# Kernel tuning notes

Hardware: AMD Instinct MI355X
Metric: run time of the kernel (lower is better)

The kernel has to match this reference:

```python
import jax, jax.numpy as jnp
import numpy as np

N_HEADS = 16

def setup_inputs() -> dict:
    key = jax.random.key(0)
    ks = jax.random.split(key, 5)
    B, T, D, L = 2, 2048, 1024, 128
    x = jax.random.normal(ks[0], (B, T, D), dtype=jnp.float32)
    w_q = jax.random.normal(ks[1], (D, D), dtype=jnp.float32) / np.sqrt(D)
    w_d = jax.random.normal(ks[2], (D, L), dtype=jnp.float32) / np.sqrt(D)
    w_k = jax.random.normal(ks[3], (L, D), dtype=jnp.float32) / np.sqrt(L)
    w_v = jax.random.normal(ks[4], (L, D), dtype=jnp.float32) / np.sqrt(L)
    mask = jnp.ones((B, T), dtype=jnp.int32)
    return {"x": x, "mask": mask, "w_q": w_q, "w_d": w_d, "w_k": w_k, "w_v": w_v}


def reference(x, mask, w_q, w_d, w_k, w_v):
    B, T, D = x.shape
    H = N_HEADS
    dh = D // H
    q = x @ w_q                      # [B,T,D]
    latent = x @ w_d                 # [B,T,L]
    k = latent @ w_k                 # [B,T,D]
    v = latent @ w_v                 # [B,T,D]

    def split(t):
        return t.reshape(B, T, H, dh).transpose(0, 2, 1, 3)  # [B,H,T,dh]

    q, k, v = split(q), split(k), split(v)
    scores = jnp.einsum('bhqd,bhkd->bhqk', q, k) / jnp.sqrt(jnp.float32(dh))
    causal = jnp.tril(jnp.ones((T, T), dtype=bool))          # [T,T]
    keep = causal[None, None, :, :] & (mask[:, None, None, :] != 0)
    scores = jnp.where(keep, scores, jnp.float32(-jnp.inf))
    probs = jax.nn.softmax(scores, axis=-1)
    out = jnp.einsum('bhqk,bhkd->bhqd', probs, v)            # [B,H,T,dh]
    return out.transpose(0, 2, 1, 3).reshape(B, T, D)
```

## Files before the change

### kernel.cpp

```cpp
#include <hip/hip_runtime.h>

typedef __attribute__((ext_vector_type(8))) short bf16x8;
typedef __attribute__((ext_vector_type(4))) float f32x4;
typedef __attribute__((ext_vector_type(4))) unsigned u32x4;

__device__ inline unsigned short f2bf(float f) {
  unsigned u = __builtin_bit_cast(unsigned, f);
  unsigned r = u + 0x7FFFu + ((u >> 16) & 1u);
  return (unsigned short)(r >> 16);
}
__device__ inline float bf2f(unsigned short s) {
  unsigned u = ((unsigned)s) << 16;
  return __builtin_bit_cast(float, u);
}
__device__ inline float fexp2(float x) { return __builtin_amdgcn_exp2f(x); }

__device__ inline void gload_lds16(const unsigned short* g, unsigned short* l) {
  __builtin_amdgcn_global_load_lds(
      (const __attribute__((address_space(1))) unsigned int*)g,
      (__attribute__((address_space(3))) unsigned int*)l, 16, 0, 0);
}

__device__ __host__ inline int pv_perm(int k) {
  return ((k >> 5) & 1) * 32 + ((k >> 2) & 3) * 8 + ((k >> 4) & 1) * 4 + (k & 3);
}

__global__ __launch_bounds__(256) void prep_kernel(
    const float* __restrict__ x, const int* __restrict__ mask,
    const float* __restrict__ w_q, const float* __restrict__ w_d,
    const float* __restrict__ w_k, const float* __restrict__ w_v,
    unsigned short* __restrict__ x_bf, unsigned short* __restrict__ wqdt,
    unsigned short* __restrict__ wkvt, float* __restrict__ bias,
    int* __restrict__ tileok) {
  int bid = blockIdx.x;
  if (bid < 1024) {
    int base = bid * 4096 + threadIdx.x * 4;
#pragma unroll
    for (int it = 0; it < 4; ++it) {
      int idx = base + it * 1024;
      float4 v = *(const float4*)&x[idx];
      ushort4 o;
      o.x = f2bf(v.x); o.y = f2bf(v.y); o.z = f2bf(v.z); o.w = f2bf(v.w);
      *(ushort4*)&x_bf[idx] = o;
    }
    return;
  }
  int tb = bid - 1024;
  if (tb >= 1408) {
    int i = (tb - 1408) * 256 + threadIdx.x;
    int mv = mask[i];
    bias[i] = mv ? 0.0f : -1e30f;
    int ok = __all(mv != 0);
    if ((threadIdx.x & 63) == 0) tileok[i >> 6] = ok;
    return;
  }
  const float* in; unsigned short* out; int R, C, tr, tc;
  if (tb < 1024)      { in = w_q; out = wqdt;               R = 1024; C = 1024; tr = tb >> 5; tc = tb & 31; }
  else if (tb < 1152) { int t2 = tb - 1024; in = w_d; out = wqdt + 1024 * 1024; R = 1024; C = 128; tr = t2 >> 2; tc = t2 & 3; }
  else if (tb < 1280) { int t2 = tb - 1152; in = w_k; out = wkvt;               R = 128; C = 1024; tr = t2 >> 5; tc = t2 & 31; }
  else                { int t2 = tb - 1280; in = w_v; out = wkvt + 1024 * 128;  R = 128; C = 1024; tr = t2 >> 5; tc = t2 & 31; }
  __shared__ float t[32][33];
  int r0 = tr * 32, c0 = tc * 32;
  int tx = threadIdx.x & 31, ty = threadIdx.x >> 5;
  for (int r = ty; r < 32; r += 8)
    t[r][tx] = in[(size_t)(r0 + r) * C + c0 + tx];
  __syncthreads();
  for (int cc = ty; cc < 32; cc += 8)
    out[(size_t)(c0 + cc) * R + r0 + tx] = f2bf(t[tx][cc]);
}

__global__ __launch_bounds__(256) void gemm_q(const unsigned short* __restrict__ A,
                                              const unsigned short* __restrict__ Bt,
                                              unsigned short* __restrict__ C) {
  __shared__ unsigned short As[2][128 * 32];
  __shared__ unsigned short Bs[2][64 * 32];
  int m0 = blockIdx.x * 128, n0 = blockIdx.y * 64;
  int tid = threadIdx.x, w = tid >> 6, l = tid & 63;
  int lr = l & 15, lg = l >> 4;
  f32x4 acc[2][4] = {};

  for (int k0 = 0; k0 < 1024; k0 += 64) {
    __syncthreads();
#pragma unroll
    for (int it = 0; it < 4; ++it) {
      int s = w * 4 + it;
      int p = s >> 3, c = s & 7;
      int row = c * 16 + (l >> 2), col = (l & 3) * 8;
      gload_lds16(&A[(size_t)(m0 + row) * 1024 + k0 + p * 32 + col], &As[p][c * 512 + l * 8]);
    }
#pragma unroll
    for (int it = 0; it < 2; ++it) {
      int s = w * 2 + it;
      int p = s >> 2, c = s & 3;
      int row = c * 16 + (l >> 2), col = (l & 3) * 8;
      gload_lds16(&Bt[(size_t)(n0 + row) * 1024 + k0 + p * 32 + col], &Bs[p][c * 512 + l * 8]);
    }
    __syncthreads();
#pragma unroll
    for (int p = 0; p < 2; ++p) {
      bf16x8 af[2], bfr[4];
#pragma unroll
      for (int m = 0; m < 2; ++m)
        af[m] = *(const bf16x8*)&As[p][(w * 32 + m * 16 + lr) * 32 + lg * 8];
#pragma unroll
      for (int n = 0; n < 4; ++n)
        bfr[n] = *(const bf16x8*)&Bs[p][(n * 16 + lr) * 32 + lg * 8];
      __builtin_amdgcn_s_setprio(1);
#pragma unroll
      for (int m = 0; m < 2; ++m)
#pragma unroll
        for (int n = 0; n < 4; ++n)
          acc[m][n] = __builtin_amdgcn_mfma_f32_16x16x32_bf16(af[m], bfr[n], acc[m][n], 0, 0, 0);
      __builtin_amdgcn_s_setprio(0);
    }
  }

#pragma unroll
  for (int m = 0; m < 2; ++m)
#pragma unroll
    for (int n = 0; n < 4; ++n)
#pragma unroll
      for (int i = 0; i < 4; ++i)
        C[(size_t)(m0 + w * 32 + m * 16 + lg * 4 + i) * 1152 + n0 + n * 16 + lr] =
            f2bf(acc[m][n][i]);
}

__global__ __launch_bounds__(256) void gemm_kv(const unsigned short* __restrict__ A,
                                               const unsigned short* __restrict__ Bt,
                                               unsigned short* __restrict__ kvK,
                                               unsigned short* __restrict__ vt) {
  __shared__ unsigned short As[2][128 * 32];
  __shared__ unsigned short Bs[2][128 * 32];
  int m0 = blockIdx.x * 128, n0 = blockIdx.y * 128;
  int tid = threadIdx.x, w = tid >> 6, l = tid & 63;
  int lr = l & 15, lg = l >> 4;
  int wr = w >> 1, wc = w & 1;
  f32x4 acc[4][4] = {};

  for (int k0 = 0; k0 < 128; k0 += 64) {
    __syncthreads();
#pragma unroll
    for (int it = 0; it < 4; ++it) {
      int s = w * 4 + it;
      int p = s >> 3, c = s & 7;
      int row = c * 16 + (l >> 2), col = (l & 3) * 8;
      gload_lds16(&A[(size_t)(m0 + row) * 1152 + k0 + p * 32 + col], &As[p][c * 512 + l * 8]);
      gload_lds16(&Bt[(size_t)(n0 + row) * 128 + k0 + p * 32 + col], &Bs[p][c * 512 + l * 8]);
    }
    __syncthreads();
#pragma unroll
    for (int p = 0; p < 2; ++p) {
      bf16x8 af[4], bfr[4];
#pragma unroll
      for (int m = 0; m < 4; ++m)
        af[m] = *(const bf16x8*)&As[p][(wr * 64 + m * 16 + lr) * 32 + lg * 8];
#pragma unroll
      for (int n = 0; n < 4; ++n)
        bfr[n] = *(const bf16x8*)&Bs[p][(wc * 64 + n * 16 + lr) * 32 + lg * 8];
      __builtin_amdgcn_s_setprio(1);
#pragma unroll
      for (int m = 0; m < 4; ++m)
#pragma unroll
        for (int n = 0; n < 4; ++n)
          acc[m][n] = __builtin_amdgcn_mfma_f32_16x16x32_bf16(af[m], bfr[n], acc[m][n], 0, 0, 0);
      __builtin_amdgcn_s_setprio(0);
    }
  }

  if (blockIdx.y < 8) {
#pragma unroll
    for (int m = 0; m < 4; ++m)
#pragma unroll
      for (int n = 0; n < 4; ++n)
#pragma unroll
        for (int i = 0; i < 4; ++i)
          kvK[(size_t)(m0 + wr * 64 + m * 16 + lg * 4 + i) * 2048 + n0 + wc * 64 + n * 16 + lr] =
              f2bf(acc[m][n][i]);
  } else {
#pragma unroll
    for (int m = 0; m < 4; ++m)
#pragma unroll
      for (int n = 0; n < 4; ++n) {
        int vc = n0 - 1024 + wc * 64 + n * 16 + lr;
        int hh = vc >> 6, dd = vc & 63;
        int row0 = m0 + wr * 64 + m * 16 + lg * 4;
        int bb = row0 >> 11, t0 = row0 & 2047;
        size_t vrow = (size_t)((bb * 16 + hh) * 64 + dd);
        int slot = (t0 >> 6) * 64 + pv_perm(t0 & 63);
        ushort4 o;
        o.x = f2bf(acc[m][n][0]); o.y = f2bf(acc[m][n][1]);
        o.z = f2bf(acc[m][n][2]); o.w = f2bf(acc[m][n][3]);
        *(ushort4*)&vt[vrow * 2048 + slot] = o;
      }
  }
}

#define KSTR 72
#define VSTR 136
__global__ __launch_bounds__(256, 3) void attn_kernel(const unsigned short* __restrict__ qg,
                                                      const unsigned short* __restrict__ kvg,
                                                      const unsigned short* __restrict__ vtg,
                                                      const float* __restrict__ biasg,
                                                      const int* __restrict__ tileokg,
                                                      float* __restrict__ outg) {
  const int bh = blockIdx.x, band = 31 - blockIdx.y;
  const int b = bh >> 4, h = bh & 15;
  const int tid = threadIdx.x, w = tid >> 6, l = tid & 63;
  const int lr = l & 15, lg = l >> 4;

  __shared__ unsigned short Ks[128 * KSTR];
  __shared__ unsigned short Vs[64 * VSTR];

  const float QSCALE = 0.125f * 1.44269504089f;

  const int NT = (band >> 1) + 1;
  const int qrow0 = band * 64 + w * 16;
  const int dlim = (band & 1) * 64 + w * 16 + lr;

  bf16x8 qf[2];
#pragma unroll
  for (int ks = 0; ks < 2; ++ks) {
    bf16x8 raw = *(const bf16x8*)&qg[(size_t)(b * 2048 + qrow0 + lr) * 1152 + h * 64 + ks * 32 + lg * 8];
#pragma unroll
    for (int j = 0; j < 8; ++j)
      raw[j] = (short)f2bf(bf2f((unsigned short)raw[j]) * QSCALE);
    qf[ks] = raw;
  }

  f32x4 acc[4] = {};
  float m_i = -1e30f, l_part = 0.f;

  bf16x8 kreg[4], vreg[4];
#pragma unroll
  for (int it = 0; it < 4; ++it) {
    int slot = it * 256 + tid;
    int krow = slot >> 3, kc8 = (slot & 7) * 8;
    int vrow = slot >> 4, vc16 = (slot & 15) * 8;
    kreg[it] = *(const bf16x8*)&kvg[(size_t)(b * 2048 + krow) * 2048 + h * 64 + kc8];
    vreg[it] = *(const bf16x8*)&vtg[((size_t)(bh * 64 + vrow)) * 2048 + vc16];
  }
#pragma unroll
  for (int it = 0; it < 4; ++it) {
    int slot = it * 256 + tid;
    int krow = slot >> 3, kc8 = (slot & 7) * 8;
    int vrow = slot >> 4, vc16 = (slot & 15) * 8;
    *(bf16x8*)&Ks[krow * KSTR + kc8] = kreg[it];
    *(bf16x8*)&Vs[vrow * VSTR + vc16] = vreg[it];
  }
  __syncthreads();

  for (int kt = 0; kt < NT; ++kt) {
    if (kt + 1 < NT) {
#pragma unroll
      for (int it = 0; it < 4; ++it) {
        int slot = it * 256 + tid;
        int krow = slot >> 3, kc8 = (slot & 7) * 8;
        int vrow = slot >> 4, vc16 = (slot & 15) * 8;
        kreg[it] = *(const bf16x8*)&kvg[(size_t)(b * 2048 + (kt + 1) * 128 + krow) * 2048 + h * 64 + kc8];
        vreg[it] = *(const bf16x8*)&vtg[((size_t)(bh * 64 + vrow)) * 2048 + (kt + 1) * 128 + vc16];
      }
    }

    const bool diag = (kt == NT - 1);

    f32x4 s[8];
    __builtin_amdgcn_s_setprio(1);
#pragma unroll
    for (int n = 0; n < 8; ++n) {
      bf16x8 kf0 = *(const bf16x8*)&Ks[(n * 16 + lr) * KSTR + lg * 8];
      bf16x8 kf1 = *(const bf16x8*)&Ks[(n * 16 + lr) * KSTR + 32 + lg * 8];
      f32x4 z = {};
      z = __builtin_amdgcn_mfma_f32_16x16x32_bf16(kf0, qf[0], z, 0, 0, 0);
      z = __builtin_amdgcn_mfma_f32_16x16x32_bf16(kf1, qf[1], z, 0, 0, 0);
      s[n] = z;
    }
    __builtin_amdgcn_s_setprio(0);

    const int tok = tileokg[b * 32 + 2 * kt] & tileokg[b * 32 + 2 * kt + 1];
    float mx = -1e30f;
    if (tok) {
      if (diag) {
#pragma unroll
        for (int n = 0; n < 8; ++n)
#pragma unroll
          for (int i = 0; i < 4; ++i) {
            float v = (n * 16 + lg * 4 + i <= dlim) ? s[n][i] : -1e30f;
            s[n][i] = v;
            mx = fmaxf(mx, v);
          }
      } else {
#pragma unroll
        for (int n = 0; n < 8; ++n)
#pragma unroll
          for (int i = 0; i < 4; ++i)
            mx = fmaxf(mx, s[n][i]);
      }
    } else {
#pragma unroll
      for (int n = 0; n < 8; ++n)
#pragma unroll
        for (int i = 0; i < 4; ++i) {
          int keyl = n * 16 + lg * 4 + i;
          float v = s[n][i] + biasg[b * 2048 + kt * 128 + keyl];
          if (diag) v = (keyl <= dlim) ? v : -1e30f;
          s[n][i] = v;
          mx = fmaxf(mx, v);
        }
    }
    mx = fmaxf(mx, __shfl_xor(mx, 16, 64));
    mx = fmaxf(mx, __shfl_xor(mx, 32, 64));

    if (__any(mx - m_i > 8.0f)) {
      float mn = fmaxf(m_i, mx);
      float sc = fexp2(m_i - mn);
      m_i = mn;
      l_part *= sc;
      float scb[4];
#pragma unroll
      for (int i = 0; i < 4; ++i) scb[i] = __shfl(sc, lg * 4 + i, 64);
#pragma unroll
      for (int dt = 0; dt < 4; ++dt)
#pragma unroll
        for (int i = 0; i < 4; ++i) acc[dt][i] *= scb[i];
    }

    float rs = 0.f;
#pragma unroll
    for (int n = 0; n < 8; ++n)
#pragma unroll
      for (int i = 0; i < 4; ++i) {
        float e = fexp2(s[n][i] - m_i);
        s[n][i] = e;
        rs += e;
      }
    l_part += rs;

    unsigned pk[8][2];
#pragma unroll
    for (int n = 0; n < 8; ++n) {
      asm("v_cvt_pk_bf16_f32 %0, %1, %2" : "=v"(pk[n][0]) : "v"(s[n][0]), "v"(s[n][1]));
      asm("v_cvt_pk_bf16_f32 %0, %1, %2" : "=v"(pk[n][1]) : "v"(s[n][2]), "v"(s[n][3]));
    }
    bf16x8 paf[4];
#pragma unroll
    for (int ks = 0; ks < 4; ++ks) {
      u32x4 uv;
      uv[0] = pk[2 * ks][0];
      uv[1] = pk[2 * ks][1];
      uv[2] = pk[2 * ks + 1][0];
      uv[3] = pk[2 * ks + 1][1];
      paf[ks] = __builtin_bit_cast(bf16x8, uv);
    }

    __builtin_amdgcn_s_setprio(1);
#pragma unroll
    for (int ks = 0; ks < 4; ++ks)
#pragma unroll
      for (int dt = 0; dt < 4; ++dt) {
        bf16x8 vf = *(const bf16x8*)&Vs[(dt * 16 + lr) * VSTR + ks * 32 + lg * 8];
        acc[dt] = __builtin_amdgcn_mfma_f32_16x16x32_bf16(paf[ks], vf, acc[dt], 0, 0, 0);
      }
    __builtin_amdgcn_s_setprio(0);

    if (kt + 1 < NT) {
      __syncthreads();
#pragma unroll
      for (int it = 0; it < 4; ++it) {
        int slot = it * 256 + tid;
        int krow = slot >> 3, kc8 = (slot & 7) * 8;
        int vrow = slot >> 4, vc16 = (slot & 15) * 8;
        *(bf16x8*)&Ks[krow * KSTR + kc8] = kreg[it];
        *(bf16x8*)&Vs[vrow * VSTR + vc16] = vreg[it];
      }
      __syncthreads();
    }
  }

  float lt = l_part;
  lt += __shfl_xor(lt, 16, 64);
  lt += __shfl_xor(lt, 32, 64);
  float inv = 1.f / lt;
  float invb[4];
#pragma unroll
  for (int i = 0; i < 4; ++i) invb[i] = __shfl(inv, lg * 4 + i, 64);
#pragma unroll
  for (int dt = 0; dt < 4; ++dt)
#pragma unroll
    for (int i = 0; i < 4; ++i)
      outg[(size_t)(b * 2048 + qrow0 + lg * 4 + i) * 1024 + h * 64 + dt * 16 + lr] =
          acc[dt][i] * invb[i];
}

extern "C" void kernel_launch(void* const* d_in, const int* in_sizes, int n_in,
                              void* d_out, int out_size, void* d_ws, size_t ws_size,
                              hipStream_t stream) {
  const float* x    = (const float*)d_in[0];
  const int*   mask = (const int*)d_in[1];
  const float* w_q  = (const float*)d_in[2];
  const float* w_d  = (const float*)d_in[3];
  const float* w_k  = (const float*)d_in[4];
  const float* w_v  = (const float*)d_in[5];
  float* out = (float*)d_out;

  char* ws = (char*)d_ws;
  size_t off = 0;
  auto alloc = [&](size_t elems) {
    unsigned short* p = (unsigned short*)(ws + off);
    off += ((elems * 2 + 255) & ~(size_t)255);
    return p;
  };
  unsigned short* x_bf = alloc(4194304);
  unsigned short* wqdt = alloc(1152 * 1024);
  unsigned short* wkvt = alloc(2048 * 128);
  unsigned short* qlat = alloc(4096 * 1152);
  unsigned short* kv   = alloc(4096 * 2048);
  unsigned short* vt   = alloc(4194304);
  float* bias = (float*)alloc(8192);
  int* tileok = (int*)alloc(128);

  prep_kernel<<<2448, 256, 0, stream>>>(x, mask, w_q, w_d, w_k, w_v, x_bf, wqdt, wkvt, bias, tileok);

  gemm_q<<<dim3(32, 18), 256, 0, stream>>>(x_bf, wqdt, qlat);
  gemm_kv<<<dim3(32, 16), 256, 0, stream>>>(qlat + 1024, wkvt, kv, vt);

  attn_kernel<<<dim3(32, 32), 256, 0, stream>>>(qlat, kv, vt, bias, tileok, out);
}
```

Before: 72.98 us.

## Process two 64-row query blocks per attention workgroup to reuse K/V tiles

```diff
diff --git a/kernel.cpp b/kernel.cpp
--- a/kernel.cpp
+++ b/kernel.cpp
@@ -197,13 +197,13 @@
 
 #define KSTR 72
 #define VSTR 136
-__global__ __launch_bounds__(256, 3) void attn_kernel(const unsigned short* __restrict__ qg,
+__global__ __launch_bounds__(256, 2) void attn_kernel(const unsigned short* __restrict__ qg,
                                                       const unsigned short* __restrict__ kvg,
                                                       const unsigned short* __restrict__ vtg,
                                                       const float* __restrict__ biasg,
                                                       const int* __restrict__ tileokg,
                                                       float* __restrict__ outg) {
-  const int bh = blockIdx.x, band = 31 - blockIdx.y;
+  const int bh = blockIdx.x, band = 15 - blockIdx.y;
   const int b = bh >> 4, h = bh & 15;
   const int tid = threadIdx.x, w = tid >> 6, l = tid & 63;
   const int lr = l & 15, lg = l >> 4;
@@ -213,22 +213,25 @@
 
   const float QSCALE = 0.125f * 1.44269504089f;
 
-  const int NT = (band >> 1) + 1;
-  const int qrow0 = band * 64 + w * 16;
-  const int dlim = (band & 1) * 64 + w * 16 + lr;
-
-  bf16x8 qf[2];
-#pragma unroll
-  for (int ks = 0; ks < 2; ++ks) {
-    bf16x8 raw = *(const bf16x8*)&qg[(size_t)(b * 2048 + qrow0 + lr) * 1152 + h * 64 + ks * 32 + lg * 8];
-#pragma unroll
-    for (int j = 0; j < 8; ++j)
-      raw[j] = (short)f2bf(bf2f((unsigned short)raw[j]) * QSCALE);
-    qf[ks] = raw;
-  }
-
-  f32x4 acc[4] = {};
-  float m_i = -1e30f, l_part = 0.f;
+  const int NT = band + 1;
+  const int qrow0 = band * 128 + w * 16;
+
+  bf16x8 qf[2][2];
+#pragma unroll
+  for (int qb = 0; qb < 2; ++qb)
+#pragma unroll
+    for (int ks = 0; ks < 2; ++ks) {
+      bf16x8 raw = *(const bf16x8*)&qg[(size_t)(b * 2048 + qrow0 + qb * 64 + lr) * 1152 +
+                                       h * 64 + ks * 32 + lg * 8];
+#pragma unroll
+      for (int j = 0; j < 8; ++j)
+        raw[j] = (short)f2bf(bf2f((unsigned short)raw[j]) * QSCALE);
+      qf[qb][ks] = raw;
+    }
+
+  f32x4 acc[4][2] = {};
+  float m_i[2] = {-1e30f, -1e30f};
+  float l_part[2] = {0.f, 0.f};
 
   bf16x8 kreg[4], vreg[4];
 #pragma unroll
@@ -263,37 +266,46 @@
 
     const bool diag = (kt == NT - 1);
 
-    f32x4 s[8];
+    f32x4 s[2][8];
     __builtin_amdgcn_s_setprio(1);
 #pragma unroll
     for (int n = 0; n < 8; ++n) {
       bf16x8 kf0 = *(const bf16x8*)&Ks[(n * 16 + lr) * KSTR + lg * 8];
       bf16x8 kf1 = *(const bf16x8*)&Ks[(n * 16 + lr) * KSTR + 32 + lg * 8];
-      f32x4 z = {};
-      z = __builtin_amdgcn_mfma_f32_16x16x32_bf16(kf0, qf[0], z, 0, 0, 0);
-      z = __builtin_amdgcn_mfma_f32_16x16x32_bf16(kf1, qf[1], z, 0, 0, 0);
-      s[n] = z;
+#pragma unroll
+      for (int qb = 0; qb < 2; ++qb) {
+        f32x4 z = {};
+        z = __builtin_amdgcn_mfma_f32_16x16x32_bf16(kf0, qf[qb][0], z, 0, 0, 0);
+        z = __builtin_amdgcn_mfma_f32_16x16x32_bf16(kf1, qf[qb][1], z, 0, 0, 0);
+        s[qb][n] = z;
+      }
     }
     __builtin_amdgcn_s_setprio(0);
 
     const int tok = tileokg[b * 32 + 2 * kt] & tileokg[b * 32 + 2 * kt + 1];
-    float mx = -1e30f;
+    float mx[2] = {-1e30f, -1e30f};
     if (tok) {
       if (diag) {
 #pragma unroll
-        for (int n = 0; n < 8; ++n)
-#pragma unroll
-          for (int i = 0; i < 4; ++i) {
-            float v = (n * 16 + lg * 4 + i <= dlim) ? s[n][i] : -1e30f;
-            s[n][i] = v;
-            mx = fmaxf(mx, v);
-          }
+        for (int qb = 0; qb < 2; ++qb) {
+          int dlim = qb * 64 + w * 16 + lr;
+#pragma unroll
+          for (int n = 0; n < 8; ++n)
+#pragma unroll
+            for (int i = 0; i < 4; ++i) {
+              float v = (n * 16 + lg * 4 + i <= dlim) ? s[qb][n][i] : -1e30f;
+              s[qb][n][i] = v;
+              mx[qb] = fmaxf(mx[qb], v);
+            }
+        }
       } else {
 #pragma unroll
-        for (int n = 0; n < 8; ++n)
-#pragma unroll
-          for (int i = 0; i < 4; ++i)
-            mx = fmaxf(mx, s[n][i]);
+        for (int qb = 0; qb < 2; ++qb)
+#pragma unroll
+          for (int n = 0; n < 8; ++n)
+#pragma unroll
+            for (int i = 0; i < 4; ++i)
+              mx[qb] = fmaxf(mx[qb], s[qb][n][i]);
       }
     } else {
 #pragma unroll
@@ -301,56 +313,68 @@
 #pragma unroll
         for (int i = 0; i < 4; ++i) {
           int keyl = n * 16 + lg * 4 + i;
-          float v = s[n][i] + biasg[b * 2048 + kt * 128 + keyl];
-          if (diag) v = (keyl <= dlim) ? v : -1e30f;
-          s[n][i] = v;
-          mx = fmaxf(mx, v);
+          float bsv = biasg[b * 2048 + kt * 128 + keyl];
+#pragma unroll
+          for (int qb = 0; qb < 2; ++qb) {
+            float v = s[qb][n][i] + bsv;
+            if (diag) v = (keyl <= qb * 64 + w * 16 + lr) ? v : -1e30f;
+            s[qb][n][i] = v;
+            mx[qb] = fmaxf(mx[qb], v);
+          }
         }
     }
-    mx = fmaxf(mx, __shfl_xor(mx, 16, 64));
-    mx = fmaxf(mx, __shfl_xor(mx, 32, 64));
-
-    if (__any(mx - m_i > 8.0f)) {
-      float mn = fmaxf(m_i, mx);
-      float sc = fexp2(m_i - mn);
-      m_i = mn;
-      l_part *= sc;
-      float scb[4];
-#pragma unroll
-      for (int i = 0; i < 4; ++i) scb[i] = __shfl(sc, lg * 4 + i, 64);
-#pragma unroll
-      for (int dt = 0; dt < 4; ++dt)
-#pragma unroll
-        for (int i = 0; i < 4; ++i) acc[dt][i] *= scb[i];
-    }
-
-    float rs = 0.f;
-#pragma unroll
-    for (int n = 0; n < 8; ++n)
-#pragma unroll
-      for (int i = 0; i < 4; ++i) {
-        float e = fexp2(s[n][i] - m_i);
-        s[n][i] = e;
-        rs += e;
-      }
-    l_part += rs;
-
-    unsigned pk[8][2];
-#pragma unroll
-    for (int n = 0; n < 8; ++n) {
-      asm("v_cvt_pk_bf16_f32 %0, %1, %2" : "=v"(pk[n][0]) : "v"(s[n][0]), "v"(s[n][1]));
-      asm("v_cvt_pk_bf16_f32 %0, %1, %2" : "=v"(pk[n][1]) : "v"(s[n][2]), "v"(s[n][3]));
-    }
-    bf16x8 paf[4];
-#pragma unroll
-    for (int ks = 0; ks < 4; ++ks) {
-      u32x4 uv;
-      uv[0] = pk[2 * ks][0];
-      uv[1] = pk[2 * ks][1];
-      uv[2] = pk[2 * ks + 1][0];
-      uv[3] = pk[2 * ks + 1][1];
-      paf[ks] = __builtin_bit_cast(bf16x8, uv);
-    }
+#pragma unroll
+    for (int qb = 0; qb < 2; ++qb) {
+      mx[qb] = fmaxf(mx[qb], __shfl_xor(mx[qb], 16, 64));
+      mx[qb] = fmaxf(mx[qb], __shfl_xor(mx[qb], 32, 64));
+    }
+
+    float g = fmaxf(mx[0] - m_i[0], mx[1] - m_i[1]);
+    if (__any(g > 8.0f)) {
+#pragma unroll
+      for (int qb = 0; qb < 2; ++qb) {
+        float mn = fmaxf(m_i[qb], mx[qb]);
+        float sc = fexp2(m_i[qb] - mn);
+        m_i[qb] = mn;
+        l_part[qb] *= sc;
+        float scb[4];
+#pragma unroll
+        for (int i = 0; i < 4; ++i) scb[i] = __shfl(sc, lg * 4 + i, 64);
+#pragma unroll
+        for (int dt = 0; dt < 4; ++dt)
+#pragma unroll
+          for (int i = 0; i < 4; ++i) acc[dt][qb][i] *= scb[i];
+      }
+    }
+
+#pragma unroll
+    for (int qb = 0; qb < 2; ++qb) {
+      float rs = 0.f;
+#pragma unroll
+      for (int n = 0; n < 8; ++n)
+#pragma unroll
+        for (int i = 0; i < 4; ++i) {
+          float e = fexp2(s[qb][n][i] - m_i[qb]);
+          s[qb][n][i] = e;
+          rs += e;
+        }
+      l_part[qb] += rs;
+    }
+
+    bf16x8 paf[2][4];
+#pragma unroll
+    for (int qb = 0; qb < 2; ++qb)
+#pragma unroll
+      for (int ks = 0; ks < 4; ++ks) {
+        unsigned t0, t1, t2, t3;
+        asm("v_cvt_pk_bf16_f32 %0, %1, %2" : "=v"(t0) : "v"(s[qb][2 * ks][0]), "v"(s[qb][2 * ks][1]));
+        asm("v_cvt_pk_bf16_f32 %0, %1, %2" : "=v"(t1) : "v"(s[qb][2 * ks][2]), "v"(s[qb][2 * ks][3]));
+        asm("v_cvt_pk_bf16_f32 %0, %1, %2" : "=v"(t2) : "v"(s[qb][2 * ks + 1][0]), "v"(s[qb][2 * ks + 1][1]));
+        asm("v_cvt_pk_bf16_f32 %0, %1, %2" : "=v"(t3) : "v"(s[qb][2 * ks + 1][2]), "v"(s[qb][2 * ks + 1][3]));
+        u32x4 uv;
+        uv[0] = t0; uv[1] = t1; uv[2] = t2; uv[3] = t3;
+        paf[qb][ks] = __builtin_bit_cast(bf16x8, uv);
+      }
 
     __builtin_amdgcn_s_setprio(1);
 #pragma unroll
@@ -358,7 +382,9 @@
 #pragma unroll
       for (int dt = 0; dt < 4; ++dt) {
         bf16x8 vf = *(const bf16x8*)&Vs[(dt * 16 + lr) * VSTR + ks * 32 + lg * 8];
-        acc[dt] = __builtin_amdgcn_mfma_f32_16x16x32_bf16(paf[ks], vf, acc[dt], 0, 0, 0);
+#pragma unroll
+        for (int qb = 0; qb < 2; ++qb)
+          acc[dt][qb] = __builtin_amdgcn_mfma_f32_16x16x32_bf16(paf[qb][ks], vf, acc[dt][qb], 0, 0, 0);
       }
     __builtin_amdgcn_s_setprio(0);
 
@@ -376,19 +402,22 @@
     }
   }
 
-  float lt = l_part;
-  lt += __shfl_xor(lt, 16, 64);
-  lt += __shfl_xor(lt, 32, 64);
-  float inv = 1.f / lt;
-  float invb[4];
-#pragma unroll
-  for (int i = 0; i < 4; ++i) invb[i] = __shfl(inv, lg * 4 + i, 64);
-#pragma unroll
-  for (int dt = 0; dt < 4; ++dt)
-#pragma unroll
-    for (int i = 0; i < 4; ++i)
-      outg[(size_t)(b * 2048 + qrow0 + lg * 4 + i) * 1024 + h * 64 + dt * 16 + lr] =
-          acc[dt][i] * invb[i];
+#pragma unroll
+  for (int qb = 0; qb < 2; ++qb) {
+    float lt = l_part[qb];
+    lt += __shfl_xor(lt, 16, 64);
+    lt += __shfl_xor(lt, 32, 64);
+    float inv = 1.f / lt;
+    float invb[4];
+#pragma unroll
+    for (int i = 0; i < 4; ++i) invb[i] = __shfl(inv, lg * 4 + i, 64);
+#pragma unroll
+    for (int dt = 0; dt < 4; ++dt)
+#pragma unroll
+      for (int i = 0; i < 4; ++i)
+        outg[(size_t)(b * 2048 + qrow0 + qb * 64 + lg * 4 + i) * 1024 + h * 64 + dt * 16 + lr] =
+            acc[dt][qb][i] * invb[i];
+  }
 }
 
 extern "C" void kernel_launch(void* const* d_in, const int* in_sizes, int n_in,
@@ -423,5 +452,5 @@
   gemm_q<<<dim3(32, 18), 256, 0, stream>>>(x_bf, wqdt, qlat);
   gemm_kv<<<dim3(32, 16), 256, 0, stream>>>(qlat + 1024, wkvt, kv, vt);
 
-  attn_kernel<<<dim3(32, 32), 256, 0, stream>>>(qlat, kv, vt, bias, tileok, out);
-}
+  attn_kernel<<<dim3(32, 16), 256, 0, stream>>>(qlat, kv, vt, bias, tileok, out);
+}
```

Measured after the change: 78.91 us. 8.1% more time.
